# Kernel optimization log

Hardware: AMD Instinct MI355X
Metric: run time of the kernel (lower is better)

## Reference

```python
import jax, jax.numpy as jnp
import numpy as np

NUM_HEADS = 8
HIDDEN = 128
MAX_NEIGHBORS = 64
BATCH = 8192


def setup_inputs() -> dict:
    key = jax.random.key(0)
    ks = jax.random.split(key, 4)
    query = jax.random.normal(ks[0], (BATCH, MAX_NEIGHBORS, HIDDEN), dtype=jnp.float32)
    value = jax.random.normal(ks[1], (BATCH, 1, HIDDEN), dtype=jnp.float32)
    # per-head Dense(hidden) weights (glorot-ish scale) + zero biases
    Wa = jax.random.normal(ks[2], (NUM_HEADS, HIDDEN, HIDDEN), dtype=jnp.float32) * (1.0 / np.sqrt(HIDDEN))
    ba = jnp.zeros((NUM_HEADS, HIDDEN), dtype=jnp.float32)
    Wo = jax.random.normal(ks[3], (NUM_HEADS * HIDDEN, HIDDEN), dtype=jnp.float32) * (1.0 / np.sqrt(NUM_HEADS * HIDDEN))
    bo = jnp.zeros((HIDDEN,), dtype=jnp.float32)
    return {"query": query, "value": value, "Wa": Wa, "ba": ba, "Wo": Wo, "bo": bo}


def reference(query, value, Wa, ba, Wo, bo):
    # query: [B, N, H], value: [B, 1, H]
    q = jnp.concatenate([query, value], axis=1)  # [B, N+1, H]
    contexts = []
    for i in range(NUM_HEADS):
        # sequential per-head projection of the running query tensor
        q = jnp.einsum('bnh,hk->bnk', q, Wa[i]) + ba[i]          # [B, N+1, H]
        e = jnp.einsum('boh,bnh->bon', value, q)                 # [B, 1, N+1]
        scores = jax.nn.softmax(e, axis=-1)                      # [B, 1, N+1]
        contexts.append(jnp.einsum('bon,bnh->boh', scores, q))   # [B, 1, H]
    ctx = jnp.concatenate(contexts, axis=-1)                     # [B, 1, num_heads*H]
    x = jnp.einsum('boc,ck->bok', ctx, Wo) + bo                  # [B, 1, H]
    return jax.nn.relu(x)
```

## Files before the change

kernel.cpp:

```cpp
#include <hip/hip_runtime.h>
#include <math.h>

#define WS_P  0
#define WS_Q0 65536
#define WS_Q1 81920
#define WS_R  98304
#define WS_WT 114688
#define WS_WU 245760
#define WS_ZT 376832
#define WS_Z0 507904
#define WS_U  524288
#define WS_PO 8912896

struct MMJob { const float* A; const float* B; float* C; float* wu; };
struct MMArgs { MMJob j[8]; };

__device__ __forceinline__ float dpp_xor1(float x) {
  return __int_as_float(__builtin_amdgcn_update_dpp(0, __float_as_int(x), 0xB1, 0xF, 0xF, false));
}
__device__ __forceinline__ float dpp_xor2(float x) {
  return __int_as_float(__builtin_amdgcn_update_dpp(0, __float_as_int(x), 0x4E, 0xF, 0xF, false));
}
__device__ __forceinline__ float dpp_xor8(float x) {
  return __int_as_float(__builtin_amdgcn_update_dpp(0, __float_as_int(x), 0x128, 0xF, 0xF, false));
}
__device__ __forceinline__ float readlane_f(float v, int n) {
  return __int_as_float(__builtin_amdgcn_readlane(__float_as_int(v), n));
}

__device__ void mm128_job(const MMJob J, const int tile, const int t, float* Al) {
  const int col = t & 127;
  const int rg = t >> 7;
  if (J.A == nullptr) {
    for (int rr = 0; rr < 16; ++rr) {
      const int r = tile * 32 + rg * 16 + rr;
      const float v = J.B[r * 128 + col];
      if (J.C) J.C[r * 128 + col] = v;
      if (J.wu) J.wu[col * 1024 + r] = v;
    }
    return;
  }
  for (int jj = 0; jj < 16; ++jj) {
    const int idx = t + jj * 256;
    Al[idx] = J.A[tile * 32 * 128 + idx];
  }
  __syncthreads();
  float acc[16];
#pragma unroll
  for (int rr = 0; rr < 16; ++rr) acc[rr] = 0.f;
  for (int h = 0; h < 128; ++h) {
    const float bv = J.B[h * 128 + col];
#pragma unroll
    for (int rr = 0; rr < 16; ++rr)
      acc[rr] = fmaf(Al[(rg * 16 + rr) * 128 + h], bv, acc[rr]);
  }
#pragma unroll
  for (int rr = 0; rr < 16; ++rr) {
    const int r = tile * 32 + rg * 16 + rr;
    if (J.C) J.C[r * 128 + col] = acc[rr];
    if (J.wu) J.wu[col * 1024 + r] = acc[rr];
  }
}

__global__ __launch_bounds__(256) void mm128_jobs(MMArgs args) {
  __shared__ float smem[4096];
  mm128_job(args.j[blockIdx.x >> 2], blockIdx.x & 3, threadIdx.x, smem);
}

__device__ void bias_z0_dev(const float* __restrict__ Wa, const float* __restrict__ ba,
                            const float* __restrict__ Wo, const float* __restrict__ bo,
                            float* __restrict__ z0, const int t, float* smem) {
  float* bt = smem;
  float* zpart = smem + 1024;
  if (t < 128) bt[t] = ba[t];
  __syncthreads();
  for (int i = 1; i < 8; ++i) {
    if (t < 128) {
      float v = ba[i * 128 + t];
      for (int h = 0; h < 128; ++h)
        v = fmaf(bt[(i - 1) * 128 + h], Wa[i * 16384 + h * 128 + t], v);
      bt[i * 128 + t] = v;
    }
    __syncthreads();
  }
  const int col = t & 127, half = t >> 7;
  float z = half ? 0.f : bo[col];
  for (int i = half * 4; i < half * 4 + 4; ++i)
    for (int h = 0; h < 128; ++h)
      z = fmaf(bt[i * 128 + h], Wo[(i * 128 + h) * 128 + col], z);
  zpart[half * 128 + col] = z;
  __syncthreads();
  if (t < 128) z0[t] = zpart[t] + zpart[128 + t];
}

__device__ void gemm_U_dev(const float* __restrict__ V, const float* __restrict__ WU,
                           float* __restrict__ U, const int bid, const int t, float* Vl) {
  const int rt = bid >> 3;
  const int ct = bid & 7;
  const int cg = t & 7;
  const int rg = t >> 3;
  const int r0 = rt * 128;
  float4 acc[4][4];
#pragma unroll
  for (int a = 0; a < 4; ++a)
#pragma unroll
    for (int c = 0; c < 4; ++c) acc[a][c] = make_float4(0.f, 0.f, 0.f, 0.f);
  for (int kc = 0; kc < 4; ++kc) {
    __syncthreads();
    {
      const int srow = t >> 3, k8 = t & 7;
#pragma unroll
      for (int pp = 0; pp < 4; ++pp) {
        const int rr = pp * 32 + srow;
        *(float4*)&Vl[rr * 33 + k8 * 4] =
            *(const float4*)&V[(size_t)(r0 + rr) * 128 + kc * 32 + k8 * 4];
      }
    }
    __syncthreads();
#pragma unroll 4
    for (int kk = 0; kk < 32; ++kk) {
      const float* wrow = WU + (size_t)(kc * 32 + kk) * 1024 + ct * 128 + cg * 16;
      const float4 w0 = *(const float4*)(wrow + 0);
      const float4 w1 = *(const float4*)(wrow + 4);
      const float4 w2 = *(const float4*)(wrow + 8);
      const float4 w3 = *(const float4*)(wrow + 12);
#pragma unroll
      for (int r = 0; r < 4; ++r) {
        const float s = Vl[(rg * 4 + r) * 33 + kk];
        acc[r][0].x = fmaf(s, w0.x, acc[r][0].x); acc[r][0].y = fmaf(s, w0.y, acc[r][0].y);
        acc[r][0].z = fmaf(s, w0.z, acc[r][0].z); acc[r][0].w = fmaf(s, w0.w, acc[r][0].w);
        acc[r][1].x = fmaf(s, w1.x, acc[r][1].x); acc[r][1].y = fmaf(s, w1.y, acc[r][1].y);
        acc[r][1].z = fmaf(s, w1.z, acc[r][1].z); acc[r][1].w = fmaf(s, w1.w, acc[r][1].w);
        acc[r][2].x = fmaf(s, w2.x, acc[r][2].x); acc[r][2].y = fmaf(s, w2.y, acc[r][2].y);
        acc[r][2].z = fmaf(s, w2.z, acc[r][2].z); acc[r][2].w = fmaf(s, w2.w, acc[r][2].w);
        acc[r][3].x = fmaf(s, w3.x, acc[r][3].x); acc[r][3].y = fmaf(s, w3.y, acc[r][3].y);
        acc[r][3].z = fmaf(s, w3.z, acc[r][3].z); acc[r][3].w = fmaf(s, w3.w, acc[r][3].w);
      }
    }
  }
#pragma unroll
  for (int r = 0; r < 4; ++r) {
    float* urow = U + (size_t)(r0 + rg * 4 + r) * 1024 + ct * 128 + cg * 16;
    *(float4*)(urow + 0) = acc[r][0];
    *(float4*)(urow + 4) = acc[r][1];
    *(float4*)(urow + 8) = acc[r][2];
    *(float4*)(urow + 12) = acc[r][3];
  }
}

__global__ __launch_bounds__(256) void k4_combo(MMArgs args,
    const float* __restrict__ V, const float* __restrict__ WU, float* __restrict__ U,
    const float* __restrict__ Wa, const float* __restrict__ ba,
    const float* __restrict__ Wo, const float* __restrict__ bo,
    float* __restrict__ z0) {
  __shared__ float smem[4224];
  const int bid = blockIdx.x;
  if (bid < 32) mm128_job(args.j[bid >> 2], bid & 3, threadIdx.x, smem);
  else if (bid < 544) gemm_U_dev(V, WU, U, bid - 32, threadIdx.x, smem);
  else bias_z0_dev(Wa, ba, Wo, bo, z0, threadIdx.x, smem);
}

__global__ __launch_bounds__(256, 4) void attn_main_k(
    const float* __restrict__ query, const float* __restrict__ value,
    float* __restrict__ U) {
  __shared__ float smem[4948];
  float* sct = smem + 4420;
  const int b = blockIdx.x;
  const int t = threadIdx.x;
  const int w = t >> 6;
  const int l = t & 63;

  const int sel1 = l & 1, sel2 = (l >> 1) & 1, sel8 = (l >> 3) & 1;
  const int g = ((l >> 2) & 1) | (((l >> 4) & 1) << 1) | (((l >> 5) & 1) << 2);
  const int myhead = 4 * sel1 + 2 * sel2 + sel8;
  const int ebase = myhead * 8 + g;

  float2 u2[8];
  {
    const float* ub = U + (size_t)b * 1024 + 2 * l;
#pragma unroll
    for (int jj = 0; jj < 8; ++jj) u2[jj] = *(const float2*)(ub + ((myhead ^ jj) << 7));
  }
  float2 q2[16];
  {
    const float* qb = query + (size_t)b * 8192 + (size_t)(w * 16) * 128 + 2 * l;
#pragma unroll
    for (int r = 0; r < 16; ++r) q2[r] = *(const float2*)(qb + r * 128);
  }
  const float2 v2 = *(const float2*)(value + (size_t)b * 128 + 2 * l);

  auto epass = [&](const float2 qv, const int n) {
    float p[8];
#pragma unroll
    for (int i = 0; i < 8; ++i) p[i] = fmaf(qv.y, u2[i].y, qv.x * u2[i].x);
    float a4[4];
#pragma unroll
    for (int i = 0; i < 4; ++i) a4[i] = p[i] + dpp_xor1(p[i + 4]);
    float a2v[2];
#pragma unroll
    for (int i = 0; i < 2; ++i) a2v[i] = a4[i] + dpp_xor2(a4[i + 2]);
    smem[n * 68 + ebase] = a2v[0] + dpp_xor8(a2v[1]);
  };
#pragma unroll
  for (int r = 0; r < 16; ++r) epass(q2[r], 16 * w + r);
  if (w == 0) epass(v2, 64);
  __syncthreads();

#pragma unroll
  for (int ii = 0; ii < 2; ++ii) {
    const int i = 2 * w + ii;
    const float4 e0 = *(const float4*)&smem[l * 68 + i * 8];
    const float4 e1 = *(const float4*)&smem[l * 68 + i * 8 + 4];
    const float4 f0 = *(const float4*)&smem[64 * 68 + i * 8];
    const float4 f1 = *(const float4*)&smem[64 * 68 + i * 8 + 4];
    const float x = ((e0.x + e0.y) + (e0.z + e0.w)) + ((e1.x + e1.y) + (e1.z + e1.w));
    const float x64 = ((f0.x + f0.y) + (f0.z + f0.w)) + ((f1.x + f1.y) + (f1.z + f1.w));
    float m = x;
    m = fmaxf(m, dpp_xor1(m));
    m = fmaxf(m, dpp_xor2(m));
    m = fmaxf(m, __shfl_xor(m, 4));
    m = fmaxf(m, dpp_xor8(m));
    m = fmaxf(m, __shfl_xor(m, 16));
    m = fmaxf(m, __shfl_xor(m, 32));
    m = fmaxf(m, x64);
    const float p = __expf(x - m);
    const float p64 = __expf(x64 - m);
    float ss = p;
    ss += dpp_xor1(ss);
    ss += dpp_xor2(ss);
    ss += __shfl_xor(ss, 4);
    ss += dpp_xor8(ss);
    ss += __shfl_xor(ss, 16);
    ss += __shfl_xor(ss, 32);
    ss += p64;
    const float inv = 1.0f / ss;
    sct[i * 66 + l] = p * inv;
    if (l == 0) sct[i * 66 + 64] = p64 * inv;
  }
  __syncthreads();

  float sc[8], c64[8];
#pragma unroll
  for (int i = 0; i < 8; ++i) sc[i] = sct[i * 66 + l];
#pragma unroll
  for (int i = 0; i < 8; ++i) c64[i] = sct[i * 66 + 64];

  float2 s2[8];
#pragma unroll
  for (int i = 0; i < 8; ++i) s2[i] = make_float2(0.f, 0.f);
#pragma unroll
  for (int r = 0; r < 16; ++r) {
    const int n = 16 * w + r;
#pragma unroll
    for (int i = 0; i < 8; ++i) {
      const float cwv = readlane_f(sc[i], n);
      s2[i].x = fmaf(cwv, q2[r].x, s2[i].x);
      s2[i].y = fmaf(cwv, q2[r].y, s2[i].y);
    }
  }
  if (w == 0) {
#pragma unroll
    for (int i = 0; i < 8; ++i) {
      s2[i].x = fmaf(c64[i], v2.x, s2[i].x);
      s2[i].y = fmaf(c64[i], v2.y, s2[i].y);
    }
  }
#pragma unroll
  for (int i = 0; i < 8; ++i)
    *(float2*)&smem[w * 1024 + i * 128 + 2 * l] = s2[i];
  __syncthreads();
  float4 acc = make_float4(0.f, 0.f, 0.f, 0.f);
#pragma unroll
  for (int w4 = 0; w4 < 4; ++w4) {
    const float4 pp = *(const float4*)&smem[w4 * 1024 + t * 4];
    acc.x += pp.x; acc.y += pp.y; acc.z += pp.z; acc.w += pp.w;
  }
  *(float4*)(U + (size_t)b * 1024 + t * 4) = acc;
}

__global__ __launch_bounds__(256) void gemm_out_k(
    const float* __restrict__ S, const float* __restrict__ Z,
    float* __restrict__ P0, float* __restrict__ PW) {
  __shared__ float STl[64 * 68];
  const int rb = blockIdx.x >> 2;
  const int kc = blockIdx.x & 3;
  const int t = threadIdx.x;
  const int rg = t >> 4;
  const int cg = t & 15;
  float4 acc[4][2];
#pragma unroll
  for (int r = 0; r < 4; ++r) {
    acc[r][0] = make_float4(0.f, 0.f, 0.f, 0.f);
    acc[r][1] = make_float4(0.f, 0.f, 0.f, 0.f);
  }
  for (int sub = 0; sub < 4; ++sub) {
    const int kb = kc * 256 + sub * 64;
    __syncthreads();
#pragma unroll
    for (int j = 0; j < 4; ++j) {
      const int i4 = t + j * 256;
      const int row = i4 >> 4, kq = i4 & 15;
      const float4 s4 = *(const float4*)&S[(size_t)(rb * 64 + row) * 1024 + kb + kq * 4];
      STl[(kq * 4 + 0) * 68 + row] = s4.x;
      STl[(kq * 4 + 1) * 68 + row] = s4.y;
      STl[(kq * 4 + 2) * 68 + row] = s4.z;
      STl[(kq * 4 + 3) * 68 + row] = s4.w;
    }
    __syncthreads();
#pragma unroll 4
    for (int k = 0; k < 64; ++k) {
      const float4 sa = *(const float4*)&STl[k * 68 + rg * 4];
      const float* zr = Z + (size_t)(kb + k) * 128 + cg * 8;
      const float4 za = *(const float4*)zr;
      const float4 zb = *(const float4*)(zr + 4);
      const float sr[4] = {sa.x, sa.y, sa.z, sa.w};
#pragma unroll
      for (int r = 0; r < 4; ++r) {
        acc[r][0].x = fmaf(sr[r], za.x, acc[r][0].x);
        acc[r][0].y = fmaf(sr[r], za.y, acc[r][0].y);
        acc[r][0].z = fmaf(sr[r], za.z, acc[r][0].z);
        acc[r][0].w = fmaf(sr[r], za.w, acc[r][0].w);
        acc[r][1].x = fmaf(sr[r], zb.x, acc[r][1].x);
        acc[r][1].y = fmaf(sr[r], zb.y, acc[r][1].y);
        acc[r][1].z = fmaf(sr[r], zb.z, acc[r][1].z);
        acc[r][1].w = fmaf(sr[r], zb.w, acc[r][1].w);
      }
    }
  }
  float* P = (kc == 0) ? P0 : (PW + (size_t)(kc - 1) * 1048576);
#pragma unroll
  for (int r = 0; r < 4; ++r) {
    float* prow = P + (size_t)(rb * 64 + rg * 4 + r) * 128 + cg * 8;
    *(float4*)(prow + 0) = acc[r][0];
    *(float4*)(prow + 4) = acc[r][1];
  }
}

__global__ __launch_bounds__(256) void reduce_relu_k(
    float* __restrict__ out, const float* __restrict__ PW,
    const float* __restrict__ z0) {
  const int idx = blockIdx.x * 256 + threadIdx.x;
  const float4 z4 = *(const float4*)&z0[(idx & 31) * 4];
  float4 a = ((const float4*)out)[idx];
  const float4 p1 = ((const float4*)(PW + 0 * 1048576))[idx];
  const float4 p2 = ((const float4*)(PW + 1 * 1048576))[idx];
  const float4 p3 = ((const float4*)(PW + 2 * 1048576))[idx];
  a.x = fmaxf(a.x + p1.x + p2.x + p3.x + z4.x, 0.f);
  a.y = fmaxf(a.y + p1.y + p2.y + p3.y + z4.y, 0.f);
  a.z = fmaxf(a.z + p1.z + p2.z + p3.z + z4.z, 0.f);
  a.w = fmaxf(a.w + p1.w + p2.w + p3.w + z4.w, 0.f);
  ((float4*)out)[idx] = a;
}

extern "C" void kernel_launch(void* const* d_in, const int* in_sizes, int n_in,
                              void* d_out, int out_size, void* d_ws, size_t ws_size,
                              hipStream_t stream) {
  const float* query = (const float*)d_in[0];
  const float* value = (const float*)d_in[1];
  const float* Wa    = (const float*)d_in[2];
  const float* ba    = (const float*)d_in[3];
  const float* Wo    = (const float*)d_in[4];
  const float* bo    = (const float*)d_in[5];
  float* ws = (float*)d_ws;
  float* P  = ws + WS_P;
  float* Q0 = ws + WS_Q0;
  float* Q1 = ws + WS_Q1;
  float* R  = ws + WS_R;
  float* WT = ws + WS_WT;
  float* WU = ws + WS_WU;
  float* ZT = ws + WS_ZT;
  float* Z0 = ws + WS_Z0;
  float* U  = ws + WS_U;
  float* PW = ws + WS_PO;

  MMArgs a1{};
  for (int j = 0; j < 4; ++j)
    a1.j[j] = MMJob{Wa + 2 * j * 16384, Wa + (2 * j + 1) * 16384, P + j * 16384, nullptr};
  mm128_jobs<<<16, 256, 0, stream>>>(a1);

  MMArgs a2{};
  a2.j[0] = MMJob{P, P + 16384, Q0, nullptr};
  a2.j[1] = MMJob{P + 2 * 16384, P + 3 * 16384, Q1, nullptr};
  a2.j[2] = MMJob{P + 2 * 16384, Wa + 6 * 16384, R, nullptr};
  mm128_jobs<<<12, 256, 0, stream>>>(a2);

  MMArgs a3{};
  a3.j[0] = MMJob{nullptr, Wa,             WT + 0 * 16384, WU + 0 * 128};
  a3.j[1] = MMJob{nullptr, P,              WT + 1 * 16384, WU + 1 * 128};
  a3.j[2] = MMJob{P,       Wa + 2 * 16384, WT + 2 * 16384, WU + 2 * 128};
  a3.j[3] = MMJob{nullptr, Q0,             WT + 3 * 16384, WU + 3 * 128};
  a3.j[4] = MMJob{Q0,      Wa + 4 * 16384, WT + 4 * 16384, WU + 4 * 128};
  a3.j[5] = MMJob{Q0,      P + 2 * 16384,  WT + 5 * 16384, WU + 5 * 128};
  a3.j[6] = MMJob{Q0,      R,              WT + 6 * 16384, WU + 6 * 128};
  a3.j[7] = MMJob{Q0,      Q1,             WT + 7 * 16384, WU + 7 * 128};
  mm128_jobs<<<32, 256, 0, stream>>>(a3);

  MMArgs a4{};
  for (int i = 0; i < 8; ++i)
    a4.j[i] = MMJob{WT + i * 16384, Wo + i * 16384, ZT + i * 16384, nullptr};
  k4_combo<<<545, 256, 0, stream>>>(a4, value, WU, U, Wa, ba, Wo, bo, Z0);

  attn_main_k<<<8192, 256, 0, stream>>>(query, value, U);

  gemm_out_k<<<512, 256, 0, stream>>>(U, ZT, (float*)d_out, PW);
  reduce_relu_k<<<1024, 256, 0, stream>>>((float*)d_out, PW, Z0);
}
```

Baseline: 220.7 us.

## Widen attention kernel to 512 threads and re-read query instead of holding it

The per-batch attention kernel now uses 8 waves of 512 threads, each handling 8 neighbor rows instead of 16. Query rows are no longer held in registers across the softmax; they are reloaded from global memory for the context accumulation, and the softmax weights are stored transposed in shared memory so they can be read as float4 instead of through readlane broadcasts. The aim is to cut register pressure and raise occupancy. The cost is a second read of query (mostly expected to hit cache), a larger shared-memory footprint, and a final reduction over 8 partial sums instead of 4.

```diff
diff --git a/kernel.cpp b/kernel.cpp
--- a/kernel.cpp
+++ b/kernel.cpp
@@ -23,9 +23,6 @@
 }
 __device__ __forceinline__ float dpp_xor8(float x) {
   return __int_as_float(__builtin_amdgcn_update_dpp(0, __float_as_int(x), 0x128, 0xF, 0xF, false));
-}
-__device__ __forceinline__ float readlane_f(float v, int n) {
-  return __int_as_float(__builtin_amdgcn_readlane(__float_as_int(v), n));
 }
 
 __device__ void mm128_job(const MMJob J, const int tile, const int t, float* Al) {
@@ -160,11 +157,11 @@
   else bias_z0_dev(Wa, ba, Wo, bo, z0, threadIdx.x, smem);
 }
 
-__global__ __launch_bounds__(256, 4) void attn_main_k(
+__global__ __launch_bounds__(512, 8) void attn_main_k(
     const float* __restrict__ query, const float* __restrict__ value,
     float* __restrict__ U) {
-  __shared__ float smem[4948];
-  float* sct = smem + 4420;
+  __shared__ float smem[8192 + 780];
+  float* sct = smem + 8192;
   const int b = blockIdx.x;
   const int t = threadIdx.x;
   const int w = t >> 6;
@@ -175,40 +172,42 @@
   const int myhead = 4 * sel1 + 2 * sel2 + sel8;
   const int ebase = myhead * 8 + g;
 
-  float2 u2[8];
   {
-    const float* ub = U + (size_t)b * 1024 + 2 * l;
-#pragma unroll
-    for (int jj = 0; jj < 8; ++jj) u2[jj] = *(const float2*)(ub + ((myhead ^ jj) << 7));
-  }
-  float2 q2[16];
+    float2 u2[8];
+    {
+      const float* ub = U + (size_t)b * 1024 + 2 * l;
+#pragma unroll
+      for (int jj = 0; jj < 8; ++jj) u2[jj] = *(const float2*)(ub + ((myhead ^ jj) << 7));
+    }
+    float2 q2[8];
+    {
+      const float* qb = query + (size_t)b * 8192 + (size_t)(w * 8) * 128 + 2 * l;
+#pragma unroll
+      for (int r = 0; r < 8; ++r) q2[r] = *(const float2*)(qb + r * 128);
+    }
+    auto epass = [&](const float2 qv, const int n) {
+      float p[8];
+#pragma unroll
+      for (int i = 0; i < 8; ++i) p[i] = fmaf(qv.y, u2[i].y, qv.x * u2[i].x);
+      float a4[4];
+#pragma unroll
+      for (int i = 0; i < 4; ++i) a4[i] = p[i] + dpp_xor1(p[i + 4]);
+      float a2v[2];
+#pragma unroll
+      for (int i = 0; i < 2; ++i) a2v[i] = a4[i] + dpp_xor2(a4[i + 2]);
+      smem[n * 68 + ebase] = a2v[0] + dpp_xor8(a2v[1]);
+    };
+#pragma unroll
+    for (int r = 0; r < 8; ++r) epass(q2[r], 8 * w + r);
+    if (w == 0) {
+      const float2 v2 = *(const float2*)(value + (size_t)b * 128 + 2 * l);
+      epass(v2, 64);
+    }
+  }
+  __syncthreads();
+
   {
-    const float* qb = query + (size_t)b * 8192 + (size_t)(w * 16) * 128 + 2 * l;
-#pragma unroll
-    for (int r = 0; r < 16; ++r) q2[r] = *(const float2*)(qb + r * 128);
-  }
-  const float2 v2 = *(const float2*)(value + (size_t)b * 128 + 2 * l);
-
-  auto epass = [&](const float2 qv, const int n) {
-    float p[8];
-#pragma unroll
-    for (int i = 0; i < 8; ++i) p[i] = fmaf(qv.y, u2[i].y, qv.x * u2[i].x);
-    float a4[4];
-#pragma unroll
-    for (int i = 0; i < 4; ++i) a4[i] = p[i] + dpp_xor1(p[i + 4]);
-    float a2v[2];
-#pragma unroll
-    for (int i = 0; i < 2; ++i) a2v[i] = a4[i] + dpp_xor2(a4[i + 2]);
-    smem[n * 68 + ebase] = a2v[0] + dpp_xor8(a2v[1]);
-  };
-#pragma unroll
-  for (int r = 0; r < 16; ++r) epass(q2[r], 16 * w + r);
-  if (w == 0) epass(v2, 64);
-  __syncthreads();
-
-#pragma unroll
-  for (int ii = 0; ii < 2; ++ii) {
-    const int i = 2 * w + ii;
+    const int i = w;
     const float4 e0 = *(const float4*)&smem[l * 68 + i * 8];
     const float4 e1 = *(const float4*)&smem[l * 68 + i * 8 + 4];
     const float4 f0 = *(const float4*)&smem[64 * 68 + i * 8];
@@ -234,48 +233,55 @@
     ss += __shfl_xor(ss, 32);
     ss += p64;
     const float inv = 1.0f / ss;
-    sct[i * 66 + l] = p * inv;
-    if (l == 0) sct[i * 66 + 64] = p64 * inv;
-  }
-  __syncthreads();
-
-  float sc[8], c64[8];
-#pragma unroll
-  for (int i = 0; i < 8; ++i) sc[i] = sct[i * 66 + l];
-#pragma unroll
-  for (int i = 0; i < 8; ++i) c64[i] = sct[i * 66 + 64];
-
-  float2 s2[8];
-#pragma unroll
-  for (int i = 0; i < 8; ++i) s2[i] = make_float2(0.f, 0.f);
-#pragma unroll
-  for (int r = 0; r < 16; ++r) {
-    const int n = 16 * w + r;
-#pragma unroll
-    for (int i = 0; i < 8; ++i) {
-      const float cwv = readlane_f(sc[i], n);
-      s2[i].x = fmaf(cwv, q2[r].x, s2[i].x);
-      s2[i].y = fmaf(cwv, q2[r].y, s2[i].y);
-    }
-  }
-  if (w == 0) {
-#pragma unroll
-    for (int i = 0; i < 8; ++i) {
-      s2[i].x = fmaf(c64[i], v2.x, s2[i].x);
-      s2[i].y = fmaf(c64[i], v2.y, s2[i].y);
-    }
-  }
-#pragma unroll
-  for (int i = 0; i < 8; ++i)
-    *(float2*)&smem[w * 1024 + i * 128 + 2 * l] = s2[i];
-  __syncthreads();
-  float4 acc = make_float4(0.f, 0.f, 0.f, 0.f);
-#pragma unroll
-  for (int w4 = 0; w4 < 4; ++w4) {
-    const float4 pp = *(const float4*)&smem[w4 * 1024 + t * 4];
-    acc.x += pp.x; acc.y += pp.y; acc.z += pp.z; acc.w += pp.w;
-  }
-  *(float4*)(U + (size_t)b * 1024 + t * 4) = acc;
+    sct[l * 12 + i] = p * inv;
+    if (l == 0) sct[64 * 12 + i] = p64 * inv;
+  }
+  __syncthreads();
+
+  {
+    float2 s2[8];
+#pragma unroll
+    for (int i = 0; i < 8; ++i) s2[i] = make_float2(0.f, 0.f);
+    const float* qb = query + (size_t)b * 8192 + (size_t)(w * 8) * 128 + 2 * l;
+#pragma unroll
+    for (int r = 0; r < 8; ++r) {
+      const int n = 8 * w + r;
+      const float2 qv = *(const float2*)(qb + r * 128);
+      const float4 c0 = *(const float4*)&sct[n * 12];
+      const float4 c1 = *(const float4*)&sct[n * 12 + 4];
+      const float cw[8] = {c0.x, c0.y, c0.z, c0.w, c1.x, c1.y, c1.z, c1.w};
+#pragma unroll
+      for (int i = 0; i < 8; ++i) {
+        s2[i].x = fmaf(cw[i], qv.x, s2[i].x);
+        s2[i].y = fmaf(cw[i], qv.y, s2[i].y);
+      }
+    }
+    if (w == 0) {
+      const float2 v2 = *(const float2*)(value + (size_t)b * 128 + 2 * l);
+      const float4 c0 = *(const float4*)&sct[64 * 12];
+      const float4 c1 = *(const float4*)&sct[64 * 12 + 4];
+      const float cw[8] = {c0.x, c0.y, c0.z, c0.w, c1.x, c1.y, c1.z, c1.w};
+#pragma unroll
+      for (int i = 0; i < 8; ++i) {
+        s2[i].x = fmaf(cw[i], v2.x, s2[i].x);
+        s2[i].y = fmaf(cw[i], v2.y, s2[i].y);
+      }
+    }
+#pragma unroll
+    for (int i = 0; i < 8; ++i)
+      *(float2*)&smem[w * 1024 + i * 128 + 2 * l] = s2[i];
+  }
+  __syncthreads();
+
+  {
+    float2 acc = make_float2(0.f, 0.f);
+#pragma unroll
+    for (int k = 0; k < 8; ++k) {
+      const float2 pp = *(const float2*)&smem[k * 1024 + 2 * t];
+      acc.x += pp.x; acc.y += pp.y;
+    }
+    *(float2*)(U + (size_t)b * 1024 + 2 * t) = acc;
+  }
 }
 
 __global__ __launch_bounds__(256) void gemm_out_k(
@@ -400,7 +406,7 @@
     a4.j[i] = MMJob{WT + i * 16384, Wo + i * 16384, ZT + i * 16384, nullptr};
   k4_combo<<<545, 256, 0, stream>>>(a4, value, WU, U, Wa, ba, Wo, bo, Z0);
 
-  attn_main_k<<<8192, 256, 0, stream>>>(query, value, U);
+  attn_main_k<<<8192, 512, 0, stream>>>(query, value, U);
 
   gemm_out_k<<<512, 256, 0, stream>>>(U, ZT, (float*)d_out, PW);
   reduce_relu_k<<<1024, 256, 0, stream>>>((float*)d_out, PW, Z0);
```

New measurement: 236.4 us. +7.1%, slower.

## Fuse output GEMM with bias+ReLU, drop split-K partial buffers

Applied to the files above, without the earlier changes.

Replaces the split-K output GEMM plus separate reduce/ReLU kernel with a single kernel where each block computes 16 full rows over the whole K dimension and applies bias and ReLU directly. This removes the partial-sum buffers' global writes and reads and one kernel launch. In exchange each thread computes only one row, so Z is reloaded from cache four times more per FMA and register reuse drops.

```diff
diff --git a/kernel.cpp b/kernel.cpp
--- a/kernel.cpp
+++ b/kernel.cpp
@@ -10,7 +10,6 @@
 #define WS_ZT 376832
 #define WS_Z0 507904
 #define WS_U  524288
-#define WS_PO 8912896
 
 struct MMJob { const float* A; const float* B; float* C; float* wu; };
 struct MMArgs { MMJob j[8]; };
@@ -278,78 +277,49 @@
   *(float4*)(U + (size_t)b * 1024 + t * 4) = acc;
 }
 
-__global__ __launch_bounds__(256) void gemm_out_k(
+__global__ __launch_bounds__(256) void gemm_out_fused(
     const float* __restrict__ S, const float* __restrict__ Z,
-    float* __restrict__ P0, float* __restrict__ PW) {
-  __shared__ float STl[64 * 68];
-  const int rb = blockIdx.x >> 2;
-  const int kc = blockIdx.x & 3;
+    const float* __restrict__ z0, float* __restrict__ out) {
+  __shared__ float STl[16 * 132];
+  const int rb = blockIdx.x;
   const int t = threadIdx.x;
-  const int rg = t >> 4;
+  const int row = t >> 4;
   const int cg = t & 15;
-  float4 acc[4][2];
-#pragma unroll
-  for (int r = 0; r < 4; ++r) {
-    acc[r][0] = make_float4(0.f, 0.f, 0.f, 0.f);
-    acc[r][1] = make_float4(0.f, 0.f, 0.f, 0.f);
-  }
-  for (int sub = 0; sub < 4; ++sub) {
-    const int kb = kc * 256 + sub * 64;
-    __syncthreads();
-#pragma unroll
-    for (int j = 0; j < 4; ++j) {
+  float4 a0 = make_float4(0.f, 0.f, 0.f, 0.f);
+  float4 a1 = make_float4(0.f, 0.f, 0.f, 0.f);
+  for (int kc = 0; kc < 8; ++kc) {
+    const int kb = kc * 128;
+    __syncthreads();
+#pragma unroll
+    for (int j = 0; j < 2; ++j) {
       const int i4 = t + j * 256;
-      const int row = i4 >> 4, kq = i4 & 15;
-      const float4 s4 = *(const float4*)&S[(size_t)(rb * 64 + row) * 1024 + kb + kq * 4];
-      STl[(kq * 4 + 0) * 68 + row] = s4.x;
-      STl[(kq * 4 + 1) * 68 + row] = s4.y;
-      STl[(kq * 4 + 2) * 68 + row] = s4.z;
-      STl[(kq * 4 + 3) * 68 + row] = s4.w;
+      const int r = i4 >> 5, k4 = i4 & 31;
+      *(float4*)&STl[r * 132 + k4 * 4] =
+          *(const float4*)&S[(size_t)(rb * 16 + r) * 1024 + kb + k4 * 4];
     }
     __syncthreads();
 #pragma unroll 4
-    for (int k = 0; k < 64; ++k) {
-      const float4 sa = *(const float4*)&STl[k * 68 + rg * 4];
-      const float* zr = Z + (size_t)(kb + k) * 128 + cg * 8;
+    for (int kk = 0; kk < 128; ++kk) {
+      const float s = STl[row * 132 + kk];
+      const float* zr = Z + (size_t)(kb + kk) * 128 + cg * 8;
       const float4 za = *(const float4*)zr;
       const float4 zb = *(const float4*)(zr + 4);
-      const float sr[4] = {sa.x, sa.y, sa.z, sa.w};
-#pragma unroll
-      for (int r = 0; r < 4; ++r) {
-        acc[r][0].x = fmaf(sr[r], za.x, acc[r][0].x);
-        acc[r][0].y = fmaf(sr[r], za.y, acc[r][0].y);
-        acc[r][0].z = fmaf(sr[r], za.z, acc[r][0].z);
-        acc[r][0].w = fmaf(sr[r], za.w, acc[r][0].w);
-        acc[r][1].x = fmaf(sr[r], zb.x, acc[r][1].x);
-        acc[r][1].y = fmaf(sr[r], zb.y, acc[r][1].y);
-        acc[r][1].z = fmaf(sr[r], zb.z, acc[r][1].z);
-        acc[r][1].w = fmaf(sr[r], zb.w, acc[r][1].w);
-      }
-    }
-  }
-  float* P = (kc == 0) ? P0 : (PW + (size_t)(kc - 1) * 1048576);
-#pragma unroll
-  for (int r = 0; r < 4; ++r) {
-    float* prow = P + (size_t)(rb * 64 + rg * 4 + r) * 128 + cg * 8;
-    *(float4*)(prow + 0) = acc[r][0];
-    *(float4*)(prow + 4) = acc[r][1];
-  }
-}
-
-__global__ __launch_bounds__(256) void reduce_relu_k(
-    float* __restrict__ out, const float* __restrict__ PW,
-    const float* __restrict__ z0) {
-  const int idx = blockIdx.x * 256 + threadIdx.x;
-  const float4 z4 = *(const float4*)&z0[(idx & 31) * 4];
-  float4 a = ((const float4*)out)[idx];
-  const float4 p1 = ((const float4*)(PW + 0 * 1048576))[idx];
-  const float4 p2 = ((const float4*)(PW + 1 * 1048576))[idx];
-  const float4 p3 = ((const float4*)(PW + 2 * 1048576))[idx];
-  a.x = fmaxf(a.x + p1.x + p2.x + p3.x + z4.x, 0.f);
-  a.y = fmaxf(a.y + p1.y + p2.y + p3.y + z4.y, 0.f);
-  a.z = fmaxf(a.z + p1.z + p2.z + p3.z + z4.z, 0.f);
-  a.w = fmaxf(a.w + p1.w + p2.w + p3.w + z4.w, 0.f);
-  ((float4*)out)[idx] = a;
+      a0.x = fmaf(s, za.x, a0.x); a0.y = fmaf(s, za.y, a0.y);
+      a0.z = fmaf(s, za.z, a0.z); a0.w = fmaf(s, za.w, a0.w);
+      a1.x = fmaf(s, zb.x, a1.x); a1.y = fmaf(s, zb.y, a1.y);
+      a1.z = fmaf(s, zb.z, a1.z); a1.w = fmaf(s, zb.w, a1.w);
+    }
+  }
+  const float4 za0 = *(const float4*)&z0[cg * 8];
+  const float4 za1 = *(const float4*)&z0[cg * 8 + 4];
+  float4 o0, o1;
+  o0.x = fmaxf(a0.x + za0.x, 0.f); o0.y = fmaxf(a0.y + za0.y, 0.f);
+  o0.z = fmaxf(a0.z + za0.z, 0.f); o0.w = fmaxf(a0.w + za0.w, 0.f);
+  o1.x = fmaxf(a1.x + za1.x, 0.f); o1.y = fmaxf(a1.y + za1.y, 0.f);
+  o1.z = fmaxf(a1.z + za1.z, 0.f); o1.w = fmaxf(a1.w + za1.w, 0.f);
+  float* orow = out + (size_t)(rb * 16 + row) * 128 + cg * 8;
+  *(float4*)(orow + 0) = o0;
+  *(float4*)(orow + 4) = o1;
 }
 
 extern "C" void kernel_launch(void* const* d_in, const int* in_sizes, int n_in,
@@ -371,7 +341,6 @@
   float* ZT = ws + WS_ZT;
   float* Z0 = ws + WS_Z0;
   float* U  = ws + WS_U;
-  float* PW = ws + WS_PO;
 
   MMArgs a1{};
   for (int j = 0; j < 4; ++j)
@@ -402,6 +371,5 @@
 
   attn_main_k<<<8192, 256, 0, stream>>>(query, value, U);
 
-  gemm_out_k<<<512, 256, 0, stream>>>(U, ZT, (float*)d_out, PW);
-  reduce_relu_k<<<1024, 256, 0, stream>>>((float*)d_out, PW, Z0);
-}
+  gemm_out_fused<<<512, 256, 0, stream>>>(U, ZT, Z0, (float*)d_out);
+}
```

New measurement: 293.3 us. 32.9% more time.
